# Kernel optimization log

Measured on AMD Instinct MI355X. Metric: run time of the kernel, lower is better.

## Reference

```python
import jax, jax.numpy as jnp
import numpy as np

B, T = 128, 512
H, E, V, NC = 1024, 1024, 32000, 10


def _unif(key, shape, fan_in):
    s = 1.0 / np.sqrt(fan_in)
    return jax.random.uniform(key, shape, minval=-s, maxval=s, dtype=jnp.float32)


def setup_inputs() -> dict:
    key = jax.random.key(0)
    ks = jax.random.split(key, 9)
    x = jax.random.randint(ks[0], (B, T), 0, V, dtype=jnp.int32)
    embed = jax.random.normal(ks[1], (V + 1, E), dtype=jnp.float32)
    Wg = _unif(ks[2], (3, E + H), E + H)
    bg = _unif(ks[3], (3,), E + H)
    Wc = _unif(ks[4], (H, E + H), E + H)
    bc = _unif(ks[5], (H,), E + H)
    Wo = _unif(ks[6], (NC, H), H)
    bo = _unif(ks[7], (NC,), H)
    return {"x": x, "embed": embed, "Wg": Wg, "bg": bg, "Wc": Wc, "bc": bc, "Wo": Wo, "bo": bo}


def reference(x, embed, Wg, bg, Wc, bc, Wo, bo):
    # alive[t] = 1 while no prefix step had sum(x[:, t]) == 0 (early-exit break)
    alive = jnp.cumprod((jnp.sum(x, axis=0) != 0).astype(jnp.float32))  # [T]
    xe = embed[x]  # [B, T, E]

    def step(carry, xt):
        h, c = carry
        xc = jnp.concatenate([xt, h], axis=1)              # [B, E+H]
        g = jax.nn.sigmoid(xc @ Wg.T + bg)                 # [B, 3]
        gi, gf, go = g[:, 0:1], g[:, 1:2], g[:, 2:3]
        Cn = gi * jnp.tanh(xc @ Wc.T + bc) + gf * c        # [B, H]
        h_new = go * jnp.tanh(Cn)
        # Faithful to source: c is NOT updated (original returns old c)
        return (h_new, c), h_new

    h0 = jnp.zeros((B, H), dtype=xe.dtype)
    c0 = jnp.zeros((B, H), dtype=xe.dtype)
    (_, _), hs = jax.lax.scan(step, (h0, c0), jnp.swapaxes(xe, 0, 1))  # hs: [T, B, H]

    mean_h = jnp.sum(hs * alive[:, None, None], axis=0) / jnp.sum(alive)  # [B, H]
    return mean_h @ Wo.T + bo  # [B, NC]
```

## Files before the change

kernel.cpp:

```cpp
#include <hip/hip_runtime.h>
#include <hip/hip_bf16.h>
#include <stdint.h>

#define B_  128
#define T_  512
#define H_  1024
#define E_  1024
#define NC_ 10
#define NT_ (B_*T_)

#define BAR_STEP  0
#define BAR_DEAD  4096

typedef __attribute__((ext_vector_type(8))) short  short8;
typedef __attribute__((ext_vector_type(4))) float  f32x4;

static __device__ __forceinline__ float bf2f(ushort u){
  union { uint u; float f; } v; v.u = ((uint)u) << 16; return v.f;
}
static __device__ __forceinline__ ushort f2bf(float f){
  union { float f; uint u; } v; v.f = f;
  uint u = v.u;
  uint lsb = (u >> 16) & 1u;
  u += 0x7fffu + lsb;
  return (ushort)(u >> 16);
}
static __device__ __forceinline__ float fsig(float x){ return 1.f / (1.f + __expf(-x)); }
static __device__ __forceinline__ float ftanh(float x){
  float e = __expf(2.f * x);
  return 1.f - 2.f / (e + 1.f);
}

#define ASYNC_COPY16(gsrc, ldsdst) \
  __builtin_amdgcn_global_load_lds((const __attribute__((address_space(1))) uint32_t*)(gsrc), \
                                   (__attribute__((address_space(3))) uint32_t*)(ldsdst), 16, 0, 0)

static __device__ __forceinline__ long long rtclock(){
  return (long long)__builtin_amdgcn_s_memrealtime();
}

__global__ __launch_bounds__(512) void k_alive(const int* __restrict__ x,
                                               float* __restrict__ alive,
                                               float* __restrict__ aliveSum){
  __shared__ float fl[T_];
  int t = threadIdx.x;
  int s = 0;
  for (int b = 0; b < B_; ++b) s += x[b*T_ + t];
  fl[t] = (s != 0) ? 1.f : 0.f;
  __syncthreads();
  if (t == 0){
    float run = 1.f, sum = 0.f;
    for (int i = 0; i < T_; ++i){ run *= fl[i]; alive[i] = run; sum += run; }
    aliveSum[0] = sum;
  }
}

__global__ __launch_bounds__(256) void k_convW(const float* __restrict__ Wc,
                                               ushort* __restrict__ Wcb){
  int idx = blockIdx.x*256 + threadIdx.x;
  if (idx < 1024*2048) Wcb[idx] = f2bf(Wc[idx]);
}

__global__ __launch_bounds__(256) void k_gather(const int* __restrict__ x,
                                                const float* __restrict__ embed,
                                                ushort* __restrict__ XB){
  size_t g = (size_t)blockIdx.x*256 + threadIdx.x;
  const size_t total = (size_t)NT_ * 128;
  for (; g < total; g += (size_t)gridDim.x*256){
    size_t row = g >> 7;
    int cj = (int)(g & 127) * 8;
    int tok = x[row];
    const float* src = embed + (size_t)tok*1024 + cj;
    float4 v0 = *(const float4*)src;
    float4 v1 = *(const float4*)(src + 4);
    uint4 o;
    o.x = (uint)f2bf(v0.x) | ((uint)f2bf(v0.y) << 16);
    o.y = (uint)f2bf(v0.z) | ((uint)f2bf(v0.w) << 16);
    o.z = (uint)f2bf(v1.x) | ((uint)f2bf(v1.y) << 16);
    o.w = (uint)f2bf(v1.z) | ((uint)f2bf(v1.w) << 16);
    *(uint4*)&XB[g*8] = o;
  }
}

__global__ __launch_bounds__(256) void k_gemmA(const ushort* __restrict__ XB,
                                               const ushort* __restrict__ Wcb,
                                               const float* __restrict__ bc,
                                               ushort* __restrict__ A2){
  __shared__ ushort As[128*64];
  __shared__ ushort Bs[128*64];
  const int bx = blockIdx.x;
  const int nt = bx & 7, mt = bx >> 3;
  const int tid = threadIdx.x, w = tid >> 6, l = tid & 63;
  const int wm = w >> 1, wn = w & 1;
  f32x4 acc[4][4];
  #pragma unroll
  for (int i = 0; i < 4; ++i)
    #pragma unroll
    for (int j = 0; j < 4; ++j) acc[i][j] = (f32x4){0.f,0.f,0.f,0.f};

  const int lrow = l >> 3, lcol = (l & 7) * 8;
  for (int kt = 0; kt < 16; ++kt){
    #pragma unroll
    for (int i = 0; i < 4; ++i){
      int cc = i*4 + w;
      const ushort* ga = XB  + (size_t)(mt*128 + cc*8 + lrow)*1024 + kt*64 + lcol;
      ASYNC_COPY16(ga, (char*)As + cc*1024);
      const ushort* gb = Wcb + (size_t)(nt*128 + cc*8 + lrow)*2048 + kt*64 + lcol;
      ASYNC_COPY16(gb, (char*)Bs + cc*1024);
    }
    __syncthreads();
    #pragma unroll
    for (int ks = 0; ks < 2; ++ks){
      short8 a[4], b[4];
      #pragma unroll
      for (int mi = 0; mi < 4; ++mi)
        a[mi] = *(const short8*)&As[(wm*64 + mi*16 + (l & 15))*64 + ks*32 + (l >> 4)*8];
      #pragma unroll
      for (int ni = 0; ni < 4; ++ni)
        b[ni] = *(const short8*)&Bs[(wn*64 + ni*16 + (l & 15))*64 + ks*32 + (l >> 4)*8];
      #pragma unroll
      for (int mi = 0; mi < 4; ++mi)
        #pragma unroll
        for (int ni = 0; ni < 4; ++ni)
          acc[mi][ni] = __builtin_amdgcn_mfma_f32_16x16x32_bf16(a[mi], b[ni], acc[mi][ni], 0, 0, 0);
    }
    __syncthreads();
  }
  const int col0 = nt*128 + wn*64;
  const int row0 = mt*128 + wm*64;
  #pragma unroll
  for (int ni = 0; ni < 4; ++ni){
    int col = col0 + ni*16 + (l & 15);
    float bias = bc[col];
    #pragma unroll
    for (int mi = 0; mi < 4; ++mi)
      #pragma unroll
      for (int r = 0; r < 4; ++r){
        int row = row0 + mi*16 + (l >> 4)*4 + r;
        int b_i = row >> 9, t_i = row & 511;
        A2[((size_t)t_i*B_ + b_i)*1024 + col] = f2bf(acc[mi][ni][r] + bias);
      }
  }
}

__global__ __launch_bounds__(256) void k_gateG(const ushort* __restrict__ XB,
                                               const float* __restrict__ Wg,
                                               const float* __restrict__ bgv,
                                               float* __restrict__ G0,
                                               float* __restrict__ G2){
  int tid = threadIdx.x, w = tid >> 6, l = tid & 63;
  size_t n = (size_t)blockIdx.x*4 + w;
  const ushort* xr = XB + n*1024;
  int k0 = l * 16;
  float s0 = 0.f, s2 = 0.f;
  #pragma unroll
  for (int h = 0; h < 2; ++h){
    short8 xv = *(const short8*)&xr[k0 + h*8];
    #pragma unroll
    for (int e = 0; e < 8; ++e){
      float xf = bf2f((ushort)xv[e]);
      s0 += xf * Wg[(size_t)0*2048 + k0 + h*8 + e];
      s2 += xf * Wg[(size_t)2*2048 + k0 + h*8 + e];
    }
  }
  for (int off = 32; off; off >>= 1){ s0 += __shfl_xor(s0, off, 64); s2 += __shfl_xor(s2, off, 64); }
  if (l == 0){
    int b_i = (int)(n >> 9), t_i = (int)(n & 511);
    G0[(size_t)t_i*B_ + b_i] = s0 + bgv[0];
    G2[(size_t)t_i*B_ + b_i] = s2 + bgv[2];
  }
}

__global__ __launch_bounds__(256, 1) void k_recur(const ushort* __restrict__ Wcb,
                                                  const float*  __restrict__ Wg,
                                                  const ushort* __restrict__ A2,
                                                  const float*  __restrict__ G0,
                                                  const float*  __restrict__ G2,
                                                  const float*  __restrict__ alive,
                                                  ushort* __restrict__ hglob,
                                                  float*  __restrict__ hsum,
                                                  uint*   __restrict__ bar){
  __shared__ ushort WhhS[32*1024];
  __shared__ ushort hS[4*16*256];
  __shared__ ushort wgS[3*1032];
  __shared__ float  upart[4][16][33];
  __shared__ float  gpart[4][16][2];

  const int blk = blockIdx.x;
  const int bg = blk & 7, oc = blk >> 3;
  const int tid = threadIdx.x, w = tid >> 6, l = tid & 63;
  const long long tstart = rtclock();

  #pragma unroll
  for (int it = 0; it < 16; ++it){
    int ch = it*256 + tid;
    int ci = ch >> 7;
    int kb = (ch & 127) * 16;
    const char* src = (const char*)Wcb + (((size_t)(oc*32 + ci)*2048 + 1024) * 2) + kb;
    uint4 v = *(const uint4*)src;
    *(uint4*)((char*)WhhS + ci*2048 + (kb ^ ((ci & 7) << 4))) = v;
  }
  for (int it = 0; it < 13; ++it){
    int idx = it*256 + tid;
    if (idx < 3096){
      int j = idx / 1032, k = idx - j*1032;
      float v = 0.f;
      if (k < 1024){
        if (j == 0)      v = Wg[(size_t)0*2048 + 1024 + k];
        else if (j == 1) v = Wg[(size_t)2*2048 + 1024 + k];
      }
      wgS[idx] = f2bf(v);
    }
  }
  __syncthreads();

  const int r_ep = tid >> 4;
  const int c0   = (tid & 15) * 2;
  const int b_ep = bg*16 + r_ep;
  const int lr   = l & 15, lk = (l >> 4) * 8;
  const int gsel = (lr == 0) ? 0 : (lr == 2 ? 2064 : 4128);
  float hs0 = 0.f, hs1 = 0.f;

  uint* flags = &bar[BAR_STEP + bg*512];
  uint* dead  = &bar[BAR_DEAD];
  const uint* myflag = &flags[((w << 3) | (l & 7)) * 16];
  bool bail = false;

  uint  av  = *(const uint*)&A2[((size_t)0*B_ + b_ep)*1024 + oc*32 + c0];
  float gx0 = G0[b_ep], gx2 = G2[b_ep];
  float au  = alive[0];

  for (int t = 0; t < T_; ++t){
    if (t > 0 && !bail){
      const uint tgt = (uint)t;
      long long t0 = rtclock();
      uint it = 0;
      while (true){
        uint v = tgt;
        if (l < 8) v = __hip_atomic_load(myflag, __ATOMIC_RELAXED, __HIP_MEMORY_SCOPE_AGENT);
        if (__all((int)(v >= tgt))) break;
        if ((++it & 63u) == 0u){
          if (__hip_atomic_load(dead, __ATOMIC_RELAXED, __HIP_MEMORY_SCOPE_AGENT)){ bail = true; break; }
          long long now = rtclock();
          if (now - t0 > 4000000LL || now - tstart > 1000000000LL){
            if (l == 0) __hip_atomic_store(dead, 1u, __ATOMIC_RELAXED, __HIP_MEMORY_SCOPE_AGENT);
            bail = true; break;
          }
        }
        __builtin_amdgcn_s_sleep(1);
      }
    }

    const ushort* hprev = hglob + (size_t)(t & 1)*B_*H_ + (size_t)bg*16*1024;
    uint4 hv[8];
    #pragma unroll
    for (int j = 0; j < 8; ++j){
      int r = j*2 + (l >> 5);
      int s = l & 31;
      const void* src = hprev + (size_t)r*1024 + w*256 + ((s ^ (r & 7)) * 8);
      asm volatile("global_load_dwordx4 %0, %1, off sc1" : "=v"(hv[j]) : "v"(src));
    }
    asm volatile("s_waitcnt vmcnt(0)" ::: "memory");
    __builtin_amdgcn_sched_barrier(0);
    #pragma unroll
    for (int j = 0; j < 8; ++j)
      *(uint4*)((char*)hS + w*8192 + j*1024 + (size_t)l*16) = hv[j];

    f32x4 uacc0 = (f32x4){0.f,0.f,0.f,0.f};
    f32x4 uacc1 = (f32x4){0.f,0.f,0.f,0.f};
    f32x4 gacc  = (f32x4){0.f,0.f,0.f,0.f};
    #pragma unroll
    for (int ks = 0; ks < 8; ++ks){
      int kbh  = (ks*32 + lk) * 2;
      int swzh = kbh ^ ((lr & 7) << 4);
      short8 a  = *(const short8*)((const char*)hS + w*8192 + lr*512 + swzh);
      int kbw  = (w*256 + ks*32 + lk) * 2;
      int swzw = kbw ^ ((lr & 7) << 4);
      short8 b0 = *(const short8*)((const char*)WhhS + lr*2048 + swzw);
      short8 b1 = *(const short8*)((const char*)WhhS + (16 + lr)*2048 + swzw);
      short8 gv = *(const short8*)((const char*)wgS + gsel + kbw);
      uacc0 = __builtin_amdgcn_mfma_f32_16x16x32_bf16(a, b0, uacc0, 0, 0, 0);
      uacc1 = __builtin_amdgcn_mfma_f32_16x16x32_bf16(a, b1, uacc1, 0, 0, 0);
      gacc  = __builtin_amdgcn_mfma_f32_16x16x32_bf16(a, gv, gacc,  0, 0, 0);
    }
    #pragma unroll
    for (int r4 = 0; r4 < 4; ++r4){
      int m = (l >> 4)*4 + r4;
      upart[w][m][lr]      = uacc0[r4];
      upart[w][m][16 + lr] = uacc1[r4];
      if (lr == 0) gpart[w][m][0] = gacc[r4];
      if (lr == 2) gpart[w][m][1] = gacc[r4];
    }
    __syncthreads();

    float u0 = upart[0][r_ep][c0]   + upart[1][r_ep][c0]   + upart[2][r_ep][c0]   + upart[3][r_ep][c0];
    float u1 = upart[0][r_ep][c0+1] + upart[1][r_ep][c0+1] + upart[2][r_ep][c0+1] + upart[3][r_ep][c0+1];
    float gp0 = gpart[0][r_ep][0] + gpart[1][r_ep][0] + gpart[2][r_ep][0] + gpart[3][r_ep][0];
    float gp2 = gpart[0][r_ep][1] + gpart[1][r_ep][1] + gpart[2][r_ep][1] + gpart[3][r_ep][1];
    float gi = fsig(gx0 + gp0);
    float go = fsig(gx2 + gp2);
    float a0 = bf2f((ushort)(av & 0xffffu));
    float a1 = bf2f((ushort)(av >> 16));
    float hn0 = go * ftanh(gi * ftanh(a0 + u0));
    float hn1 = go * ftanh(gi * ftanh(a1 + u1));
    hs0 += au * hn0;
    hs1 += au * hn1;
    uint hv2 = (uint)f2bf(hn0) | ((uint)f2bf(hn1) << 16);
    uint* hdst = (uint*)&hglob[(size_t)((t + 1) & 1)*B_*H_ + (size_t)b_ep*1024 + oc*32 + c0];
    __hip_atomic_store(hdst, hv2, __ATOMIC_RELAXED, __HIP_MEMORY_SCOPE_AGENT);

    int tn = (t < T_-1) ? t + 1 : t;
    av  = *(const uint*)&A2[((size_t)tn*B_ + b_ep)*1024 + oc*32 + c0];
    gx0 = G0[(size_t)tn*B_ + b_ep];
    gx2 = G2[(size_t)tn*B_ + b_ep];
    au  = alive[tn];

    __syncthreads();
    if (tid == 0 && t < T_-1)
      __hip_atomic_store(&flags[oc*16], (uint)(t + 1), __ATOMIC_RELAXED, __HIP_MEMORY_SCOPE_AGENT);
  }

  hsum[(size_t)b_ep*1024 + oc*32 + c0]     = hs0;
  hsum[(size_t)b_ep*1024 + oc*32 + c0 + 1] = hs1;
}

__global__ __launch_bounds__(256) void k_out(const float* __restrict__ hsum,
                                             const float* __restrict__ Wo,
                                             const float* __restrict__ bo,
                                             const float* __restrict__ aliveSum,
                                             float* __restrict__ out){
  __shared__ float accs[NC_];
  int b = blockIdx.x, tid = threadIdx.x;
  if (tid < NC_) accs[tid] = 0.f;
  __syncthreads();
  int k0 = tid * 4;
  float4 hv = *(const float4*)&hsum[(size_t)b*1024 + k0];
  float part[NC_];
  #pragma unroll
  for (int c = 0; c < NC_; ++c){
    const float* wr = Wo + (size_t)c*1024 + k0;
    part[c] = hv.x*wr[0] + hv.y*wr[1] + hv.z*wr[2] + hv.w*wr[3];
  }
  #pragma unroll
  for (int c = 0; c < NC_; ++c){
    float v = part[c];
    for (int off = 32; off; off >>= 1) v += __shfl_xor(v, off, 64);
    if ((tid & 63) == 0) atomicAdd(&accs[c], v);
  }
  __syncthreads();
  if (tid < NC_) out[b*NC_ + tid] = accs[tid] / aliveSum[0] + bo[tid];
}

extern "C" void kernel_launch(void* const* d_in, const int* in_sizes, int n_in,
                              void* d_out, int out_size, void* d_ws, size_t ws_size,
                              hipStream_t stream){
  const int*   x     = (const int*)  d_in[0];
  const float* embed = (const float*)d_in[1];
  const float* Wg    = (const float*)d_in[2];
  const float* bg    = (const float*)d_in[3];
  const float* Wc    = (const float*)d_in[4];
  const float* bc    = (const float*)d_in[5];
  const float* Wo    = (const float*)d_in[6];
  const float* bo    = (const float*)d_in[7];
  float* out = (float*)d_out;

  char* p = (char*)d_ws;
  ushort* XB    = (ushort*)p;  p += (size_t)NT_*1024*2;
  ushort* A2    = (ushort*)p;  p += (size_t)NT_*1024*2;
  ushort* Wcb   = (ushort*)p;  p += (size_t)1024*2048*2;
  float*  G0    = (float*)p;   p += (size_t)NT_*4;
  float*  G2    = (float*)p;   p += (size_t)NT_*4;
  ushort* hglob = (ushort*)p;  p += (size_t)2*B_*H_*2;
  float*  hsum  = (float*)p;   p += (size_t)B_*H_*4;
  float*  alive = (float*)p;   p += (size_t)T_*4;
  float*  aliveSum = (float*)p; p += 256;
  uint*   bar   = (uint*)p;    p += 64*1024;

  (void)ws_size; (void)in_sizes; (void)n_in; (void)out_size;

  hipMemsetAsync(hglob, 0, (size_t)B_*H_*2, stream);
  hipMemsetAsync(bar,   0, 64*1024, stream);

  k_alive <<<1,    512, 0, stream>>>(x, alive, aliveSum);
  k_convW <<<8192, 256, 0, stream>>>(Wc, Wcb);
  k_gather<<<4096, 256, 0, stream>>>(x, embed, XB);
  k_gemmA <<<4096, 256, 0, stream>>>(XB, Wcb, bc, A2);
  k_gateG <<<16384,256, 0, stream>>>(XB, Wg, bg, G0, G2);

  k_recur<<<256, 256, 0, stream>>>(Wcb, Wg, A2, G0, G2, alive, hglob, hsum, bar);

  k_out<<<B_, 256, 0, stream>>>(hsum, Wo, bo, aliveSum, out);
}
```

Before: 1.752 ms.

## Replace flag barrier with canary-polled per-timestep hidden state buffer

The recurrence kernel no longer publishes per-step flags behind a block-wide sync. Each step writes h into its own slot of a full [T,B,H] buffer (reusing the XB workspace) that was pre-filled with an 0xFFFF canary, and consumers spin on the h data itself until no canary remains. This removes one __syncthreads and the flag round-trip per step, and double-buffers the shared partial sums to avoid the WAR hazard. The cost is an extra ~128MB memset before the kernel, and the canary can collide with a real bf16 pair equal to 0xFFFF (a NaN pattern). Timeout thresholds are also tightened.

```diff
diff --git a/kernel.cpp b/kernel.cpp
--- a/kernel.cpp
+++ b/kernel.cpp
@@ -9,8 +9,8 @@
 #define NC_ 10
 #define NT_ (B_*T_)
 
-#define BAR_STEP  0
-#define BAR_DEAD  4096
+#define BAR_DEAD  0
+#define CANARY    0xFFFFFFFFu
 
 typedef __attribute__((ext_vector_type(8))) short  short8;
 typedef __attribute__((ext_vector_type(4))) float  f32x4;
@@ -177,14 +177,14 @@
                                                   const float*  __restrict__ G0,
                                                   const float*  __restrict__ G2,
                                                   const float*  __restrict__ alive,
-                                                  ushort* __restrict__ hglob,
+                                                  ushort* __restrict__ hT,
                                                   float*  __restrict__ hsum,
                                                   uint*   __restrict__ bar){
   __shared__ ushort WhhS[32*1024];
   __shared__ ushort hS[4*16*256];
   __shared__ ushort wgS[3*1032];
-  __shared__ float  upart[4][16][33];
-  __shared__ float  gpart[4][16][2];
+  __shared__ float  upart[2][4][16][33];
+  __shared__ float  gpart[2][4][16][2];
 
   const int blk = blockIdx.x;
   const int bg = blk & 7, oc = blk >> 3;
@@ -221,9 +221,7 @@
   const int gsel = (lr == 0) ? 0 : (lr == 2 ? 2064 : 4128);
   float hs0 = 0.f, hs1 = 0.f;
 
-  uint* flags = &bar[BAR_STEP + bg*512];
-  uint* dead  = &bar[BAR_DEAD];
-  const uint* myflag = &flags[((w << 3) | (l & 7)) * 16];
+  uint* dead = &bar[BAR_DEAD];
   bool bail = false;
 
   uint  av  = *(const uint*)&A2[((size_t)0*B_ + b_ep)*1024 + oc*32 + c0];
@@ -231,41 +229,53 @@
   float au  = alive[0];
 
   for (int t = 0; t < T_; ++t){
-    if (t > 0 && !bail){
-      const uint tgt = (uint)t;
+    const ushort* hprev = hT + (size_t)t*(B_*H_) + (size_t)bg*16*1024;
+    const char* ap[8];
+    #pragma unroll
+    for (int j = 0; j < 8; ++j){
+      int r = j*2 + (l >> 5);
+      int s = l & 31;
+      ap[j] = (const char*)(hprev + (size_t)r*1024 + w*256 + ((s ^ (r & 7)) * 8));
+    }
+    uint4 hv[8];
+    #pragma unroll
+    for (int j = 0; j < 8; ++j)
+      asm volatile("global_load_dwordx4 %0, %1, off sc1" : "=v"(hv[j]) : "v"(ap[j]));
+    asm volatile("s_waitcnt vmcnt(0)" ::: "memory");
+    uint pend = 0;
+    #pragma unroll
+    for (int j = 0; j < 8; ++j)
+      if (hv[j].x == CANARY || hv[j].y == CANARY || hv[j].z == CANARY || hv[j].w == CANARY)
+        pend |= (1u << j);
+    if (!bail && __any((int)(pend != 0u))){
       long long t0 = rtclock();
       uint it = 0;
-      while (true){
-        uint v = tgt;
-        if (l < 8) v = __hip_atomic_load(myflag, __ATOMIC_RELAXED, __HIP_MEMORY_SCOPE_AGENT);
-        if (__all((int)(v >= tgt))) break;
-        if ((++it & 63u) == 0u){
+      while (__any((int)(pend != 0u))){
+        #pragma unroll
+        for (int j = 0; j < 8; ++j)
+          if (pend & (1u << j))
+            asm volatile("global_load_dwordx4 %0, %1, off sc1" : "=v"(hv[j]) : "v"(ap[j]));
+        asm volatile("s_waitcnt vmcnt(0)" ::: "memory");
+        #pragma unroll
+        for (int j = 0; j < 8; ++j)
+          if ((pend & (1u << j)) &&
+              !(hv[j].x == CANARY || hv[j].y == CANARY || hv[j].z == CANARY || hv[j].w == CANARY))
+            pend &= ~(1u << j);
+        if ((++it & 15u) == 0u){
           if (__hip_atomic_load(dead, __ATOMIC_RELAXED, __HIP_MEMORY_SCOPE_AGENT)){ bail = true; break; }
           long long now = rtclock();
-          if (now - t0 > 4000000LL || now - tstart > 1000000000LL){
-            if (l == 0) __hip_atomic_store(dead, 1u, __ATOMIC_RELAXED, __HIP_MEMORY_SCOPE_AGENT);
+          if (now - t0 > 200000LL || now - tstart > 30000000LL){
+            if (tid == 0) __hip_atomic_store(dead, 1u, __ATOMIC_RELAXED, __HIP_MEMORY_SCOPE_AGENT);
             bail = true; break;
           }
         }
-        __builtin_amdgcn_s_sleep(1);
       }
     }
-
-    const ushort* hprev = hglob + (size_t)(t & 1)*B_*H_ + (size_t)bg*16*1024;
-    uint4 hv[8];
-    #pragma unroll
-    for (int j = 0; j < 8; ++j){
-      int r = j*2 + (l >> 5);
-      int s = l & 31;
-      const void* src = hprev + (size_t)r*1024 + w*256 + ((s ^ (r & 7)) * 8);
-      asm volatile("global_load_dwordx4 %0, %1, off sc1" : "=v"(hv[j]) : "v"(src));
-    }
-    asm volatile("s_waitcnt vmcnt(0)" ::: "memory");
-    __builtin_amdgcn_sched_barrier(0);
     #pragma unroll
     for (int j = 0; j < 8; ++j)
       *(uint4*)((char*)hS + w*8192 + j*1024 + (size_t)l*16) = hv[j];
 
+    const int p = t & 1;
     f32x4 uacc0 = (f32x4){0.f,0.f,0.f,0.f};
     f32x4 uacc1 = (f32x4){0.f,0.f,0.f,0.f};
     f32x4 gacc  = (f32x4){0.f,0.f,0.f,0.f};
@@ -286,17 +296,17 @@
     #pragma unroll
     for (int r4 = 0; r4 < 4; ++r4){
       int m = (l >> 4)*4 + r4;
-      upart[w][m][lr]      = uacc0[r4];
-      upart[w][m][16 + lr] = uacc1[r4];
-      if (lr == 0) gpart[w][m][0] = gacc[r4];
-      if (lr == 2) gpart[w][m][1] = gacc[r4];
+      upart[p][w][m][lr]      = uacc0[r4];
+      upart[p][w][m][16 + lr] = uacc1[r4];
+      if (lr == 0) gpart[p][w][m][0] = gacc[r4];
+      if (lr == 2) gpart[p][w][m][1] = gacc[r4];
     }
     __syncthreads();
 
-    float u0 = upart[0][r_ep][c0]   + upart[1][r_ep][c0]   + upart[2][r_ep][c0]   + upart[3][r_ep][c0];
-    float u1 = upart[0][r_ep][c0+1] + upart[1][r_ep][c0+1] + upart[2][r_ep][c0+1] + upart[3][r_ep][c0+1];
-    float gp0 = gpart[0][r_ep][0] + gpart[1][r_ep][0] + gpart[2][r_ep][0] + gpart[3][r_ep][0];
-    float gp2 = gpart[0][r_ep][1] + gpart[1][r_ep][1] + gpart[2][r_ep][1] + gpart[3][r_ep][1];
+    float u0 = upart[p][0][r_ep][c0]   + upart[p][1][r_ep][c0]   + upart[p][2][r_ep][c0]   + upart[p][3][r_ep][c0];
+    float u1 = upart[p][0][r_ep][c0+1] + upart[p][1][r_ep][c0+1] + upart[p][2][r_ep][c0+1] + upart[p][3][r_ep][c0+1];
+    float gp0 = gpart[p][0][r_ep][0] + gpart[p][1][r_ep][0] + gpart[p][2][r_ep][0] + gpart[p][3][r_ep][0];
+    float gp2 = gpart[p][0][r_ep][1] + gpart[p][1][r_ep][1] + gpart[p][2][r_ep][1] + gpart[p][3][r_ep][1];
     float gi = fsig(gx0 + gp0);
     float go = fsig(gx2 + gp2);
     float a0 = bf2f((ushort)(av & 0xffffu));
@@ -306,7 +316,7 @@
     hs0 += au * hn0;
     hs1 += au * hn1;
     uint hv2 = (uint)f2bf(hn0) | ((uint)f2bf(hn1) << 16);
-    uint* hdst = (uint*)&hglob[(size_t)((t + 1) & 1)*B_*H_ + (size_t)b_ep*1024 + oc*32 + c0];
+    uint* hdst = (uint*)&hT[(size_t)((t + 1) & 511)*(B_*H_) + (size_t)b_ep*1024 + oc*32 + c0];
     __hip_atomic_store(hdst, hv2, __ATOMIC_RELAXED, __HIP_MEMORY_SCOPE_AGENT);
 
     int tn = (t < T_-1) ? t + 1 : t;
@@ -314,10 +324,6 @@
     gx0 = G0[(size_t)tn*B_ + b_ep];
     gx2 = G2[(size_t)tn*B_ + b_ep];
     au  = alive[tn];
-
-    __syncthreads();
-    if (tid == 0 && t < T_-1)
-      __hip_atomic_store(&flags[oc*16], (uint)(t + 1), __ATOMIC_RELAXED, __HIP_MEMORY_SCOPE_AGENT);
   }
 
   hsum[(size_t)b_ep*1024 + oc*32 + c0]     = hs0;
@@ -365,21 +371,20 @@
   float* out = (float*)d_out;
 
   char* p = (char*)d_ws;
-  ushort* XB    = (ushort*)p;  p += (size_t)NT_*1024*2;
+  ushort* XB    = (ushort*)p;
+  ushort* hT    = (ushort*)p;  p += (size_t)NT_*1024*2;
   ushort* A2    = (ushort*)p;  p += (size_t)NT_*1024*2;
   ushort* Wcb   = (ushort*)p;  p += (size_t)1024*2048*2;
   float*  G0    = (float*)p;   p += (size_t)NT_*4;
   float*  G2    = (float*)p;   p += (size_t)NT_*4;
-  ushort* hglob = (ushort*)p;  p += (size_t)2*B_*H_*2;
   float*  hsum  = (float*)p;   p += (size_t)B_*H_*4;
   float*  alive = (float*)p;   p += (size_t)T_*4;
   float*  aliveSum = (float*)p; p += 256;
-  uint*   bar   = (uint*)p;    p += 64*1024;
+  uint*   bar   = (uint*)p;    p += 4*1024;
 
   (void)ws_size; (void)in_sizes; (void)n_in; (void)out_size;
 
-  hipMemsetAsync(hglob, 0, (size_t)B_*H_*2, stream);
-  hipMemsetAsync(bar,   0, 64*1024, stream);
+  hipMemsetAsync(bar, 0, 4*1024, stream);
 
   k_alive <<<1,    512, 0, stream>>>(x, alive, aliveSum);
   k_convW <<<8192, 256, 0, stream>>>(Wc, Wcb);
@@ -387,7 +392,10 @@
   k_gemmA <<<4096, 256, 0, stream>>>(XB, Wcb, bc, A2);
   k_gateG <<<16384,256, 0, stream>>>(XB, Wg, bg, G0, G2);
 
-  k_recur<<<256, 256, 0, stream>>>(Wcb, Wg, A2, G0, G2, alive, hglob, hsum, bar);
+  hipMemsetAsync(hT, 0, (size_t)B_*H_*2, stream);
+  hipMemsetAsync(hT + (size_t)B_*H_, 0xFF, (size_t)511*B_*H_*2, stream);
+
+  k_recur<<<256, 256, 0, stream>>>(Wcb, Wg, A2, G0, G2, alive, hT, hsum, bar);
 
   k_out<<<B_, 256, 0, stream>>>(hsum, Wo, bo, aliveSum, out);
 }
```

Result: slower. 2.333 ms (+33.2%).

## Signal per-wave step flags and double-buffer partial sums to drop trailing barrier

Applied to the files above, without the earlier changes.

Each wave now publishes its own step flag once its hidden-state stores have drained, replacing the block-wide barrier followed by a single per-block flag. Consumers poll 32 per-wave flags, one per lane, instead of 8 block flags. The upart/gpart reduction buffers are double-buffered by step parity, so the next step's writes cannot race readers even without the trailing __syncthreads. The LDS and global hidden-state swizzle widens from 8 to 16 rows to reduce bank conflicts. The cost is more flag traffic and more polling lanes per wave.

```diff
diff --git a/kernel.cpp b/kernel.cpp
--- a/kernel.cpp
+++ b/kernel.cpp
@@ -9,8 +9,8 @@
 #define NC_ 10
 #define NT_ (B_*T_)
 
-#define BAR_STEP  0
-#define BAR_DEAD  4096
+#define BAR_DEAD  0
+#define BAR_FLAGS 256
 
 typedef __attribute__((ext_vector_type(8))) short  short8;
 typedef __attribute__((ext_vector_type(4))) float  f32x4;
@@ -183,8 +183,8 @@
   __shared__ ushort WhhS[32*1024];
   __shared__ ushort hS[4*16*256];
   __shared__ ushort wgS[3*1032];
-  __shared__ float  upart[4][16][33];
-  __shared__ float  gpart[4][16][2];
+  __shared__ float  upart[2][4][16][33];
+  __shared__ float  gpart[2][4][16][2];
 
   const int blk = blockIdx.x;
   const int bg = blk & 7, oc = blk >> 3;
@@ -198,7 +198,7 @@
     int kb = (ch & 127) * 16;
     const char* src = (const char*)Wcb + (((size_t)(oc*32 + ci)*2048 + 1024) * 2) + kb;
     uint4 v = *(const uint4*)src;
-    *(uint4*)((char*)WhhS + ci*2048 + (kb ^ ((ci & 7) << 4))) = v;
+    *(uint4*)((char*)WhhS + ci*2048 + (kb ^ ((ci & 15) << 4))) = v;
   }
   for (int it = 0; it < 13; ++it){
     int idx = it*256 + tid;
@@ -221,9 +221,10 @@
   const int gsel = (lr == 0) ? 0 : (lr == 2 ? 2064 : 4128);
   float hs0 = 0.f, hs1 = 0.f;
 
-  uint* flags = &bar[BAR_STEP + bg*512];
   uint* dead  = &bar[BAR_DEAD];
-  const uint* myflag = &flags[((w << 3) | (l & 7)) * 16];
+  uint* flags = &bar[BAR_FLAGS + bg*2048];
+  const uint* myflag = &flags[(((w << 3) | (l >> 2)) * 4 + (l & 3)) * 16];
+  uint* sigflag = &flags[((oc * 4) + w) * 16];
   bool bail = false;
 
   uint  av  = *(const uint*)&A2[((size_t)0*B_ + b_ep)*1024 + oc*32 + c0];
@@ -237,7 +238,7 @@
       uint it = 0;
       while (true){
         uint v = tgt;
-        if (l < 8) v = __hip_atomic_load(myflag, __ATOMIC_RELAXED, __HIP_MEMORY_SCOPE_AGENT);
+        if (l < 32) v = __hip_atomic_load(myflag, __ATOMIC_RELAXED, __HIP_MEMORY_SCOPE_AGENT);
         if (__all((int)(v >= tgt))) break;
         if ((++it & 63u) == 0u){
           if (__hip_atomic_load(dead, __ATOMIC_RELAXED, __HIP_MEMORY_SCOPE_AGENT)){ bail = true; break; }
@@ -257,7 +258,7 @@
     for (int j = 0; j < 8; ++j){
       int r = j*2 + (l >> 5);
       int s = l & 31;
-      const void* src = hprev + (size_t)r*1024 + w*256 + ((s ^ (r & 7)) * 8);
+      const void* src = hprev + (size_t)r*1024 + w*256 + ((s ^ (r & 15)) * 8);
       asm volatile("global_load_dwordx4 %0, %1, off sc1" : "=v"(hv[j]) : "v"(src));
     }
     asm volatile("s_waitcnt vmcnt(0)" ::: "memory");
@@ -266,16 +267,17 @@
     for (int j = 0; j < 8; ++j)
       *(uint4*)((char*)hS + w*8192 + j*1024 + (size_t)l*16) = hv[j];
 
+    const int p = t & 1;
     f32x4 uacc0 = (f32x4){0.f,0.f,0.f,0.f};
     f32x4 uacc1 = (f32x4){0.f,0.f,0.f,0.f};
     f32x4 gacc  = (f32x4){0.f,0.f,0.f,0.f};
     #pragma unroll
     for (int ks = 0; ks < 8; ++ks){
       int kbh  = (ks*32 + lk) * 2;
-      int swzh = kbh ^ ((lr & 7) << 4);
+      int swzh = kbh ^ ((lr & 15) << 4);
       short8 a  = *(const short8*)((const char*)hS + w*8192 + lr*512 + swzh);
       int kbw  = (w*256 + ks*32 + lk) * 2;
-      int swzw = kbw ^ ((lr & 7) << 4);
+      int swzw = kbw ^ ((lr & 15) << 4);
       short8 b0 = *(const short8*)((const char*)WhhS + lr*2048 + swzw);
       short8 b1 = *(const short8*)((const char*)WhhS + (16 + lr)*2048 + swzw);
       short8 gv = *(const short8*)((const char*)wgS + gsel + kbw);
@@ -286,17 +288,17 @@
     #pragma unroll
     for (int r4 = 0; r4 < 4; ++r4){
       int m = (l >> 4)*4 + r4;
-      upart[w][m][lr]      = uacc0[r4];
-      upart[w][m][16 + lr] = uacc1[r4];
-      if (lr == 0) gpart[w][m][0] = gacc[r4];
-      if (lr == 2) gpart[w][m][1] = gacc[r4];
+      upart[p][w][m][lr]      = uacc0[r4];
+      upart[p][w][m][16 + lr] = uacc1[r4];
+      if (lr == 0) gpart[p][w][m][0] = gacc[r4];
+      if (lr == 2) gpart[p][w][m][1] = gacc[r4];
     }
     __syncthreads();
 
-    float u0 = upart[0][r_ep][c0]   + upart[1][r_ep][c0]   + upart[2][r_ep][c0]   + upart[3][r_ep][c0];
-    float u1 = upart[0][r_ep][c0+1] + upart[1][r_ep][c0+1] + upart[2][r_ep][c0+1] + upart[3][r_ep][c0+1];
-    float gp0 = gpart[0][r_ep][0] + gpart[1][r_ep][0] + gpart[2][r_ep][0] + gpart[3][r_ep][0];
-    float gp2 = gpart[0][r_ep][1] + gpart[1][r_ep][1] + gpart[2][r_ep][1] + gpart[3][r_ep][1];
+    float u0 = upart[p][0][r_ep][c0]   + upart[p][1][r_ep][c0]   + upart[p][2][r_ep][c0]   + upart[p][3][r_ep][c0];
+    float u1 = upart[p][0][r_ep][c0+1] + upart[p][1][r_ep][c0+1] + upart[p][2][r_ep][c0+1] + upart[p][3][r_ep][c0+1];
+    float gp0 = gpart[p][0][r_ep][0] + gpart[p][1][r_ep][0] + gpart[p][2][r_ep][0] + gpart[p][3][r_ep][0];
+    float gp2 = gpart[p][0][r_ep][1] + gpart[p][1][r_ep][1] + gpart[p][2][r_ep][1] + gpart[p][3][r_ep][1];
     float gi = fsig(gx0 + gp0);
     float go = fsig(gx2 + gp2);
     float a0 = bf2f((ushort)(av & 0xffffu));
@@ -309,15 +311,15 @@
     uint* hdst = (uint*)&hglob[(size_t)((t + 1) & 1)*B_*H_ + (size_t)b_ep*1024 + oc*32 + c0];
     __hip_atomic_store(hdst, hv2, __ATOMIC_RELAXED, __HIP_MEMORY_SCOPE_AGENT);
 
+    asm volatile("s_waitcnt vmcnt(0)" ::: "memory");
+    if (l == 0 && t < T_-1)
+      __hip_atomic_store(sigflag, (uint)(t + 1), __ATOMIC_RELAXED, __HIP_MEMORY_SCOPE_AGENT);
+
     int tn = (t < T_-1) ? t + 1 : t;
     av  = *(const uint*)&A2[((size_t)tn*B_ + b_ep)*1024 + oc*32 + c0];
     gx0 = G0[(size_t)tn*B_ + b_ep];
     gx2 = G2[(size_t)tn*B_ + b_ep];
     au  = alive[tn];
-
-    __syncthreads();
-    if (tid == 0 && t < T_-1)
-      __hip_atomic_store(&flags[oc*16], (uint)(t + 1), __ATOMIC_RELAXED, __HIP_MEMORY_SCOPE_AGENT);
   }
 
   hsum[(size_t)b_ep*1024 + oc*32 + c0]     = hs0;
@@ -374,12 +376,12 @@
   float*  hsum  = (float*)p;   p += (size_t)B_*H_*4;
   float*  alive = (float*)p;   p += (size_t)T_*4;
   float*  aliveSum = (float*)p; p += 256;
-  uint*   bar   = (uint*)p;    p += 64*1024;
+  uint*   bar   = (uint*)p;    p += 128*1024;
 
   (void)ws_size; (void)in_sizes; (void)n_in; (void)out_size;
 
   hipMemsetAsync(hglob, 0, (size_t)B_*H_*2, stream);
-  hipMemsetAsync(bar,   0, 64*1024, stream);
+  hipMemsetAsync(bar,   0, 128*1024, stream);
 
   k_alive <<<1,    512, 0, stream>>>(x, alive, aliveSum);
   k_convW <<<8192, 256, 0, stream>>>(Wc, Wcb);
```

Result: slower. 2.083 ms (+18.9%).
